# Kernel optimization log

Hardware: AMD Instinct MI355X
Metric: run time of the kernel (lower is better)

The kernel has to match this reference:

```python
import jax, jax.numpy as jnp
import numpy as np

H, W = 512, 512
K = 10
N_ACTIONS = 8
HID1, HID2, HIDP = 32, 64, 32
# 8-neighborhood directions (i_dot, j_dot), as in env.DIRS
DIRS = [(-1, -1), (-1, 0), (-1, 1), (0, -1), (0, 1), (1, -1), (1, 0), (1, 1)]


def setup_inputs() -> dict:
    key = jax.random.key(0)
    ks = jax.random.split(key, 16)
    n_state = H * W
    w = lambda k, shape: (jax.random.normal(k, shape, dtype=jnp.float32) * 0.02)
    return {
        "x": jax.random.uniform(ks[0], (3, H, W), dtype=jnp.float32),
        "pos": jax.random.randint(ks[1], (2,), 0, H, dtype=jnp.int32),
        "W1": w(ks[2], (HID1, 3 * n_state)), "b1": jnp.zeros((HID1,), jnp.float32),
        "W2": w(ks[3], (HID2, HID1)), "b2": jnp.zeros((HID2,), jnp.float32),
        "Wro": w(ks[4], (n_state, HID2)), "bro": jnp.zeros((n_state,), jnp.float32),
        "Wri": w(ks[5], (n_state, HID2)), "bri": jnp.zeros((n_state,), jnp.float32),
        "Wp": w(ks[6], (n_state, HID2)), "bp": jnp.zeros((n_state,), jnp.float32),
        "Wpol": w(ks[7], (HIDP, 4 * n_state)), "bpol": jnp.zeros((HIDP,), jnp.float32),
        "Whead": w(ks[8], (N_ACTIONS, HIDP)), "bhead": jnp.zeros((N_ACTIONS,), jnp.float32),
    }


def reference(x, pos, W1, b1, W2, b2, Wro, bro, Wri, bri, Wp, bp, Wpol, bpol, Whead, bhead):
    state = x.reshape(-1)  # (3*H*W,)
    h = jax.nn.relu(W1 @ state + b1)
    h = jax.nn.relu(W2 @ h + b2)
    r_out = jax.nn.sigmoid(Wro @ h + bro).reshape(H, W)
    r_in = jax.nn.sigmoid(Wri @ h + bri).reshape(H, W)
    p = jax.nn.sigmoid(Wp @ h + bp).reshape(H, W)

    p_pad = jnp.pad(p, 1)
    rin_pad = jnp.pad(r_in, 1)
    rout_pad = jnp.pad(r_out, 1)

    def step(v, _):
        v_pad = jnp.pad(v, 1)  # (H+2, W+2)
        cands = []
        for i_dot, j_dot in DIRS:
            xs = j_dot + 1  # note: original code uses j_dot along axis 0
            ys = i_dot + 1
            cands.append(
                v_pad[xs:xs + H, ys:ys + W] * p_pad[xs:xs + H, ys:ys + W]
                + rin_pad[xs:xs + H, ys:ys + W] - rout_pad[xs:xs + H, ys:ys + W]
            )
        return jnp.max(jnp.stack(cands, 0), axis=0), None

    v, _ = jax.lax.scan(step, jnp.zeros((H, W), jnp.float32), None, length=K)

    inp_pol = jnp.concatenate([v.reshape(-1), state])  # (4*H*W,)
    logits = Whead @ jax.nn.relu(Wpol @ inp_pol + bpol) + bhead
    action_prob = jax.nn.softmax(logits, axis=-1)
    state_value = v[pos[0], pos[1]]
    return action_prob, state_value
```

## Files before the change

kernel.cpp:

```cpp
#include <hip/hip_runtime.h>

#define HW 512
#define NSTATE (HW * HW)
#define NC4_X 196608
#define NC4_POLROW 262144
#define NC4_V 65536

#define CH4 1024
#define NCH_X 192

#define WS_PART1 0
#define WS_PARTP 6144
#define WS_H2 14336
#define WS_DRO 16384
#define WS_DRI 278528
#define WS_DP 540672
#define WS_V 802816

#define SGB __builtin_amdgcn_sched_group_barrier

typedef float f4v __attribute__((ext_vector_type(4)));

__device__ __forceinline__ float wred(float a) {
  a += __shfl_xor(a, 32);
  a += __shfl_xor(a, 16);
  a += __shfl_xor(a, 8);
  a += __shfl_xor(a, 4);
  a += __shfl_xor(a, 2);
  a += __shfl_xor(a, 1);
  return a;
}

__device__ __forceinline__ float span_dot(const float4* __restrict__ wp,
                                          const float4* __restrict__ xp) {
  float acc = 0.f;
#pragma unroll
  for (int bt = 0; bt < 2; ++bt) {
    float4 w[8], xv[8];
#pragma unroll
    for (int j = 0; j < 8; ++j) w[j] = wp[bt * 512 + j * 64];
#pragma unroll
    for (int j = 0; j < 8; ++j) xv[j] = xp[bt * 512 + j * 64];
    SGB(0x020, 16, 0);
#pragma unroll
    for (int j = 0; j < 8; ++j)
      acc += w[j].x * xv[j].x + w[j].y * xv[j].y + w[j].z * xv[j].z +
             w[j].w * xv[j].w;
  }
  return acc;
}

__global__ __launch_bounds__(256) void mv_w1(const float4* __restrict__ W1,
                                             const float4* __restrict__ x,
                                             float* __restrict__ part1) {
  int b = blockIdx.x;
  int row = b / 48, cb = b - row * 48;
  int tid = threadIdx.x, wave = tid >> 6, lane = tid & 63;
  int ch = cb * 4 + wave;
  const float4* __restrict__ wp =
      W1 + (size_t)row * NC4_X + (size_t)ch * CH4 + lane;
  const float4* __restrict__ xp = x + (size_t)ch * CH4 + lane;
  float acc = span_dot(wp, xp);
  acc = wred(acc);
  if (lane == 0) part1[ch * 32 + row] = acc;
}

__global__ __launch_bounds__(1024) void finish_h(
    const float* __restrict__ partials, const float* __restrict__ b1,
    const float* __restrict__ W2, const float* __restrict__ b2,
    float* __restrict__ h2out) {
  __shared__ float red[32][32];
  __shared__ float h1[32];
  int tid = threadIdx.x;
  int row = tid & 31, grp = tid >> 5;
  float s = 0.f;
  for (int b = grp; b < NCH_X; b += 32) s += partials[b * 32 + row];
  red[grp][row] = s;
  __syncthreads();
  if (tid < 32) {
    float t = b1[tid];
    for (int g = 0; g < 32; ++g) t += red[g][tid];
    h1[tid] = fmaxf(t, 0.f);
  }
  __syncthreads();
  if (tid < 64) {
    float t = b2[tid];
    for (int k = 0; k < 32; ++k) t += W2[tid * 32 + k] * h1[k];
    h2out[tid] = fmaxf(t, 0.f);
  }
}

__device__ __forceinline__ void issue16(const float4* __restrict__ wp,
                                        f4v* w) {
  const float* a0 = (const float*)(wp);
  const float* a1 = (const float*)(wp + 256);
  const float* a2 = (const float*)(wp + 512);
  const float* a3 = (const float*)(wp + 768);
  asm volatile(
      "global_load_dwordx4 %0, %16, off nt\n\t"
      "global_load_dwordx4 %1, %16, off offset:1024 nt\n\t"
      "global_load_dwordx4 %2, %16, off offset:2048 nt\n\t"
      "global_load_dwordx4 %3, %16, off offset:3072 nt\n\t"
      "global_load_dwordx4 %4, %17, off nt\n\t"
      "global_load_dwordx4 %5, %17, off offset:1024 nt\n\t"
      "global_load_dwordx4 %6, %17, off offset:2048 nt\n\t"
      "global_load_dwordx4 %7, %17, off offset:3072 nt\n\t"
      "global_load_dwordx4 %8, %18, off nt\n\t"
      "global_load_dwordx4 %9, %18, off offset:1024 nt\n\t"
      "global_load_dwordx4 %10, %18, off offset:2048 nt\n\t"
      "global_load_dwordx4 %11, %18, off offset:3072 nt\n\t"
      "global_load_dwordx4 %12, %19, off nt\n\t"
      "global_load_dwordx4 %13, %19, off offset:1024 nt\n\t"
      "global_load_dwordx4 %14, %19, off offset:2048 nt\n\t"
      "global_load_dwordx4 %15, %19, off offset:3072 nt"
      : "=&v"(w[0]), "=&v"(w[1]), "=&v"(w[2]), "=&v"(w[3]), "=&v"(w[4]),
        "=&v"(w[5]), "=&v"(w[6]), "=&v"(w[7]), "=&v"(w[8]), "=&v"(w[9]),
        "=&v"(w[10]), "=&v"(w[11]), "=&v"(w[12]), "=&v"(w[13]), "=&v"(w[14]),
        "=&v"(w[15])
      : "v"(a0), "v"(a1), "v"(a2), "v"(a3)
      : "memory");
}

__device__ __forceinline__ void consume16(const f4v* w, float4 h4, int wave,
                                          int lane, float (*dots)[64],
                                          float* __restrict__ Dst) {
  float part[16];
#pragma unroll
  for (int j = 0; j < 16; ++j)
    part[j] = w[j][0] * h4.x + w[j][1] * h4.y + w[j][2] * h4.z + w[j][3] * h4.w;
#pragma unroll
  for (int j = 0; j < 16; ++j) {
    part[j] += __shfl_xor(part[j], 8);
    part[j] += __shfl_xor(part[j], 4);
    part[j] += __shfl_xor(part[j], 2);
    part[j] += __shfl_xor(part[j], 1);
  }
  int k = lane & 15, grp = lane >> 4;
  if (k == 0) {
#pragma unroll
    for (int j = 0; j < 16; ++j) dots[wave][j * 4 + grp] = part[j];
  }
  asm volatile("s_waitcnt lgkmcnt(0)" ::: "memory");
  __builtin_amdgcn_sched_barrier(0);
  Dst[lane] = dots[wave][lane];
}

#define VMW16 do { asm volatile("s_waitcnt vmcnt(16)" ::: "memory"); \
                   __builtin_amdgcn_sched_barrier(0); } while (0)
#define VMW0 do { asm volatile("s_waitcnt vmcnt(0)" ::: "memory"); \
                  __builtin_amdgcn_sched_barrier(0); } while (0)

__global__ __launch_bounds__(256, 2) void rop_part(
    const float4* __restrict__ Wro4, const float4* __restrict__ Wri4,
    const float4* __restrict__ Wp4, const float* __restrict__ h2,
    float* __restrict__ dro, float* __restrict__ dri,
    float* __restrict__ dp) {
  __shared__ float dots[4][64];
  int tid = threadIdx.x, wave = tid >> 6, lane = tid & 63;
  int gw = blockIdx.x * 4 + wave;
  float4 h4 = ((const float4*)h2)[lane & 15];
  const float4* __restrict__ p0 = Wro4 + (size_t)gw * CH4 + lane;
  const float4* __restrict__ p1 = Wri4 + (size_t)gw * CH4 + lane;
  const float4* __restrict__ p2 = Wp4 + (size_t)gw * CH4 + lane;
  f4v A[16], B[16];
  issue16(p0, A);
  issue16(p1, B);
  VMW16;
  consume16(A, h4, wave, lane, dots, dro + (size_t)gw * 64);
  issue16(p2, A);
  VMW16;
  consume16(B, h4, wave, lane, dots, dri + (size_t)gw * 64);
  VMW0;
  consume16(A, h4, wave, lane, dots, dp + (size_t)gw * 64);
}

#define VTILE 16
#define VHALO 10
#define ULW 44
#define ULH 38
__device__ __forceinline__ void row_win(const float* __restrict__ r,
                                        float e[6]) {
  float4 L = *reinterpret_cast<const float4*>(r - 4);
  float4 M = *reinterpret_cast<const float4*>(r);
  float4 R = *reinterpret_cast<const float4*>(r + 4);
  e[0] = L.w; e[1] = M.x; e[2] = M.y; e[3] = M.z; e[4] = M.w; e[5] = R.x;
}
__global__ __launch_bounds__(384) void valiter_kernel(
    const float* __restrict__ dro, const float* __restrict__ dri,
    const float* __restrict__ dp, const float* __restrict__ bro,
    const float* __restrict__ bri, const float* __restrict__ bp,
    float* __restrict__ vout) {
  __shared__ float ua[ULH * ULW];
  __shared__ float ub[ULH * ULW];
  int tid = threadIdx.x;
  int blk = blockIdx.x;
  int ti = blk >> 5, tj = blk & 31;
  for (int idx = tid; idx < ULH * ULW; idx += 384) {
    ua[idx] = 0.f;
    ub[idx] = 0.f;
  }
  int i = tid / 9, j4 = tid - i * 9;
  bool active = (i < 36);
  int cb = 4 + 4 * j4;
  float pp[4], rr[4];
  if (active) {
    int gi = ti * VTILE - VHALO + i;
    int gj0 = tj * VTILE - VHALO + 4 * j4;
#pragma unroll
    for (int k = 0; k < 4; ++k) {
      int gj = gj0 + k;
      bool ok = (gi >= 0) & (gi < HW) & (gj >= 0) & (gj < HW);
      if (ok) {
        int g = gi * HW + gj;
        float sro = 1.f / (1.f + __expf(-(dro[g] + bro[g])));
        float sri = 1.f / (1.f + __expf(-(dri[g] + bri[g])));
        pp[k] = 1.f / (1.f + __expf(-(dp[g] + bp[g])));
        rr[k] = sri - sro;
      } else {
        pp[k] = 0.f;
        rr[k] = 0.f;
      }
    }
  }
  __syncthreads();
  if (active) {
    *reinterpret_cast<float4*>(&ua[(i + 1) * ULW + cb]) =
        make_float4(rr[0], rr[1], rr[2], rr[3]);
  }
  __syncthreads();
  float* src = ua;
  float* dst = ub;
  for (int q = 0; q < 9; ++q) {
    int lo = q + 1, hi = 35 - q;
    if (active && i >= lo && i < hi && (4 * j4 + 4) > lo && (4 * j4) < hi) {
      float eA[6], eB[6], eC[6];
      row_win(src + i * ULW + cb, eA);
      row_win(src + (i + 1) * ULW + cb, eB);
      row_win(src + (i + 2) * ULW + cb, eC);
      float res[4];
#pragma unroll
      for (int k = 0; k < 4; ++k) {
        float a = fmaxf(fmaxf(eA[k], eA[k + 1]), eA[k + 2]);
        float c = fmaxf(fmaxf(eC[k], eC[k + 1]), eC[k + 2]);
        float b = fmaxf(eB[k], eB[k + 2]);
        float m = fmaxf(fmaxf(a, c), b);
        res[k] = m * pp[k] + rr[k];
      }
      *reinterpret_cast<float4*>(&dst[(i + 1) * ULW + cb]) =
          make_float4(res[0], res[1], res[2], res[3]);
    }
    __syncthreads();
    float* t_ = src;
    src = dst;
    dst = t_;
  }
  if (active && i >= 10 && i < 26 && (4 * j4 + 4) > 10 && (4 * j4) < 26) {
    float eA[6], eB[6], eC[6];
    row_win(src + i * ULW + cb, eA);
    row_win(src + (i + 1) * ULW + cb, eB);
    row_win(src + (i + 2) * ULW + cb, eC);
#pragma unroll
    for (int k = 0; k < 4; ++k) {
      int cj = 4 * j4 + k;
      if (cj >= 10 && cj < 26) {
        float a = fmaxf(fmaxf(eA[k], eA[k + 1]), eA[k + 2]);
        float c = fmaxf(fmaxf(eC[k], eC[k + 1]), eC[k + 2]);
        float b = fmaxf(eB[k], eB[k + 2]);
        float m = fmaxf(fmaxf(a, c), b);
        vout[(ti * VTILE + i - 10) * HW + tj * VTILE + cj - 10] = m;
      }
    }
  }
}

__global__ __launch_bounds__(256) void mv_pol(const float4* __restrict__ Wpol,
                                              const float4* __restrict__ x,
                                              const float4* __restrict__ v,
                                              float* __restrict__ partP) {
  int b = blockIdx.x;
  int tid = threadIdx.x, wave = tid >> 6, lane = tid & 63;
  int f = b * 4 + wave;
  int row = f >> 8, rc = f & 255;
  const float4* __restrict__ wp = Wpol + (size_t)f * CH4 + lane;
  const float4* __restrict__ xp =
      (rc < 64) ? (v + (size_t)rc * CH4 + lane)
                : (x + (size_t)(rc - 64) * CH4 + lane);
  float acc = span_dot(wp, xp);
  acc = wred(acc);
  if (lane == 0) partP[rc * 32 + row] = acc;
}

__global__ __launch_bounds__(1024) void finish_pol(
    const float* __restrict__ partP, const float* __restrict__ bpol,
    const float* __restrict__ Whead, const float* __restrict__ bhead,
    const float* __restrict__ v, const int* __restrict__ pos,
    float* __restrict__ out) {
  __shared__ float red[32][32];
  __shared__ float hp[32];
  __shared__ float logits[8];
  int tid = threadIdx.x;
  int row = tid & 31, grp = tid >> 5;
  float s = 0.f;
  for (int b = grp; b < 256; b += 32) s += partP[b * 32 + row];
  red[grp][row] = s;
  __syncthreads();
  if (tid < 32) {
    float t = bpol[tid];
    for (int g = 0; g < 32; ++g) t += red[g][tid];
    hp[tid] = fmaxf(t, 0.f);
  }
  __syncthreads();
  if (tid < 8) {
    float t = bhead[tid];
    for (int k = 0; k < 32; ++k) t += Whead[tid * 32 + k] * hp[k];
    logits[tid] = t;
  }
  __syncthreads();
  if (tid == 0) {
    float mx = logits[0];
    for (int j = 1; j < 8; ++j) mx = fmaxf(mx, logits[j]);
    float e[8], sum = 0.f;
    for (int j = 0; j < 8; ++j) {
      e[j] = __expf(logits[j] - mx);
      sum += e[j];
    }
    for (int j = 0; j < 8; ++j) out[j] = e[j] / sum;
    out[8] = v[pos[0] * HW + pos[1]];
  }
}

extern "C" void kernel_launch(void* const* d_in, const int* in_sizes, int n_in,
                              void* d_out, int out_size, void* d_ws,
                              size_t ws_size, hipStream_t stream) {
  const float* x = (const float*)d_in[0];
  const int* pos = (const int*)d_in[1];
  const float* W1 = (const float*)d_in[2];
  const float* b1 = (const float*)d_in[3];
  const float* W2 = (const float*)d_in[4];
  const float* b2 = (const float*)d_in[5];
  const float* Wro = (const float*)d_in[6];
  const float* bro = (const float*)d_in[7];
  const float* Wri = (const float*)d_in[8];
  const float* bri = (const float*)d_in[9];
  const float* Wp = (const float*)d_in[10];
  const float* bp = (const float*)d_in[11];
  const float* Wpol = (const float*)d_in[12];
  const float* bpol = (const float*)d_in[13];
  const float* Whead = (const float*)d_in[14];
  const float* bhead = (const float*)d_in[15];
  float* ws = (float*)d_ws;
  float* out = (float*)d_out;

  float* part1 = ws + WS_PART1;
  float* partP = ws + WS_PARTP;
  float* h2 = ws + WS_H2;
  float* drob = ws + WS_DRO;
  float* drib = ws + WS_DRI;
  float* dpb = ws + WS_DP;
  float* vbuf = ws + WS_V;

  mv_w1<<<1536, 256, 0, stream>>>((const float4*)W1, (const float4*)x, part1);
  finish_h<<<1, 1024, 0, stream>>>(part1, b1, W2, b2, h2);
  rop_part<<<1024, 256, 0, stream>>>((const float4*)Wro, (const float4*)Wri,
                                     (const float4*)Wp, h2, drob, drib, dpb);
  valiter_kernel<<<1024, 384, 0, stream>>>(drob, drib, dpb, bro, bri, bp,
                                           vbuf);
  mv_pol<<<2048, 256, 0, stream>>>((const float4*)Wpol, (const float4*)x,
                                   (const float4*)vbuf, partP);
  finish_pol<<<1, 1024, 0, stream>>>(partP, bpol, Whead, bhead, vbuf, pos,
                                     out);
}
```

Baseline: 105.1 us.

## Split policy matvec by input, fuse x-part into rop kernel with sigmoid epilogue

The policy matvec's state (x) portion does not depend on the value iteration, so it now runs in the same launch as the Wro/Wri/Wp matvec, interleaved by block index. Only the v-dependent quarter runs after value iteration. The sigmoids and bias adds move into the rop kernel epilogue, which writes only p and r_in-r_out. Value iteration therefore reads two halo-overlapping planes instead of six and skips repeated exp work on halo cells. The combined kernel mixes two workloads with different register and occupancy profiles.

```diff
diff --git a/kernel.cpp b/kernel.cpp
--- a/kernel.cpp
+++ b/kernel.cpp
@@ -8,14 +8,14 @@
 
 #define CH4 1024
 #define NCH_X 192
+#define NCH_V 64
 
 #define WS_PART1 0
 #define WS_PARTP 6144
 #define WS_H2 14336
-#define WS_DRO 16384
-#define WS_DRI 278528
-#define WS_DP 540672
-#define WS_V 802816
+#define WS_P 14400
+#define WS_RD (WS_P + NSTATE)
+#define WS_V (WS_RD + NSTATE)
 
 #define SGB __builtin_amdgcn_sched_group_barrier
 
@@ -122,8 +122,8 @@
 }
 
 __device__ __forceinline__ void consume16(const f4v* w, float4 h4, int wave,
-                                          int lane, float (*dots)[64],
-                                          float* __restrict__ Dst) {
+                                          int m, int lane,
+                                          float (*dots)[3][64]) {
   float part[16];
 #pragma unroll
   for (int j = 0; j < 16; ++j)
@@ -138,11 +138,8 @@
   int k = lane & 15, grp = lane >> 4;
   if (k == 0) {
 #pragma unroll
-    for (int j = 0; j < 16; ++j) dots[wave][j * 4 + grp] = part[j];
-  }
-  asm volatile("s_waitcnt lgkmcnt(0)" ::: "memory");
-  __builtin_amdgcn_sched_barrier(0);
-  Dst[lane] = dots[wave][lane];
+    for (int j = 0; j < 16; ++j) dots[wave][m][j * 4 + grp] = part[j];
+  }
 }
 
 #define VMW16 do { asm volatile("s_waitcnt vmcnt(16)" ::: "memory"); \
@@ -150,14 +147,30 @@
 #define VMW0 do { asm volatile("s_waitcnt vmcnt(0)" ::: "memory"); \
                   __builtin_amdgcn_sched_barrier(0); } while (0)
 
-__global__ __launch_bounds__(256, 2) void rop_part(
+__global__ __launch_bounds__(256, 2) void ropx(
     const float4* __restrict__ Wro4, const float4* __restrict__ Wri4,
     const float4* __restrict__ Wp4, const float* __restrict__ h2,
-    float* __restrict__ dro, float* __restrict__ dri,
-    float* __restrict__ dp) {
-  __shared__ float dots[4][64];
+    const float* __restrict__ bro, const float* __restrict__ bri,
+    const float* __restrict__ bp, float* __restrict__ p_out,
+    float* __restrict__ rd_out, const float4* __restrict__ Wpol,
+    const float4* __restrict__ x, float* __restrict__ partP) {
+  __shared__ float dots[4][3][64];
   int tid = threadIdx.x, wave = tid >> 6, lane = tid & 63;
-  int gw = blockIdx.x * 4 + wave;
+  int b5 = blockIdx.x / 5, m5 = blockIdx.x - b5 * 5;
+  if (m5 >= 2) {
+    int xblk = b5 * 3 + (m5 - 2);
+    int row = xblk / 48, cb = xblk - row * 48;
+    int ch = cb * 4 + wave;
+    const float4* __restrict__ wp =
+        Wpol + (size_t)row * NC4_POLROW + NC4_V + (size_t)ch * CH4 + lane;
+    const float4* __restrict__ xp = x + (size_t)ch * CH4 + lane;
+    float acc = span_dot(wp, xp);
+    acc = wred(acc);
+    if (lane == 0) partP[(64 + ch) * 32 + row] = acc;
+    return;
+  }
+  int rblk = b5 * 2 + m5;
+  int gw = rblk * 4 + wave;
   float4 h4 = ((const float4*)h2)[lane & 15];
   const float4* __restrict__ p0 = Wro4 + (size_t)gw * CH4 + lane;
   const float4* __restrict__ p1 = Wri4 + (size_t)gw * CH4 + lane;
@@ -166,12 +179,23 @@
   issue16(p0, A);
   issue16(p1, B);
   VMW16;
-  consume16(A, h4, wave, lane, dots, dro + (size_t)gw * 64);
+  consume16(A, h4, wave, 0, lane, dots);
   issue16(p2, A);
   VMW16;
-  consume16(B, h4, wave, lane, dots, dri + (size_t)gw * 64);
+  consume16(B, h4, wave, 1, lane, dots);
   VMW0;
-  consume16(A, h4, wave, lane, dots, dp + (size_t)gw * 64);
+  consume16(A, h4, wave, 2, lane, dots);
+  asm volatile("s_waitcnt lgkmcnt(0)" ::: "memory");
+  __builtin_amdgcn_sched_barrier(0);
+  int o = gw * 64 + lane;
+  float dro = dots[wave][0][lane] + bro[o];
+  float dri = dots[wave][1][lane] + bri[o];
+  float dp = dots[wave][2][lane] + bp[o];
+  float sro = 1.f / (1.f + __expf(-dro));
+  float sri = 1.f / (1.f + __expf(-dri));
+  float pv = 1.f / (1.f + __expf(-dp));
+  p_out[o] = pv;
+  rd_out[o] = sri - sro;
 }
 
 #define VTILE 16
@@ -186,9 +210,7 @@
   e[0] = L.w; e[1] = M.x; e[2] = M.y; e[3] = M.z; e[4] = M.w; e[5] = R.x;
 }
 __global__ __launch_bounds__(384) void valiter_kernel(
-    const float* __restrict__ dro, const float* __restrict__ dri,
-    const float* __restrict__ dp, const float* __restrict__ bro,
-    const float* __restrict__ bri, const float* __restrict__ bp,
+    const float* __restrict__ p, const float* __restrict__ rd,
     float* __restrict__ vout) {
   __shared__ float ua[ULH * ULW];
   __shared__ float ub[ULH * ULW];
@@ -210,16 +232,9 @@
     for (int k = 0; k < 4; ++k) {
       int gj = gj0 + k;
       bool ok = (gi >= 0) & (gi < HW) & (gj >= 0) & (gj < HW);
-      if (ok) {
-        int g = gi * HW + gj;
-        float sro = 1.f / (1.f + __expf(-(dro[g] + bro[g])));
-        float sri = 1.f / (1.f + __expf(-(dri[g] + bri[g])));
-        pp[k] = 1.f / (1.f + __expf(-(dp[g] + bp[g])));
-        rr[k] = sri - sro;
-      } else {
-        pp[k] = 0.f;
-        rr[k] = 0.f;
-      }
+      int gidx = gi * HW + gj;
+      pp[k] = ok ? p[gidx] : 0.f;
+      rr[k] = ok ? rd[gidx] : 0.f;
     }
   }
   __syncthreads();
@@ -273,21 +288,19 @@
   }
 }
 
-__global__ __launch_bounds__(256) void mv_pol(const float4* __restrict__ Wpol,
-                                              const float4* __restrict__ x,
-                                              const float4* __restrict__ v,
-                                              float* __restrict__ partP) {
+__global__ __launch_bounds__(256) void mv_polv(const float4* __restrict__ Wpol,
+                                               const float4* __restrict__ v,
+                                               float* __restrict__ partP) {
   int b = blockIdx.x;
+  int row = b / 16, cb = b - row * 16;
   int tid = threadIdx.x, wave = tid >> 6, lane = tid & 63;
-  int f = b * 4 + wave;
-  int row = f >> 8, rc = f & 255;
-  const float4* __restrict__ wp = Wpol + (size_t)f * CH4 + lane;
-  const float4* __restrict__ xp =
-      (rc < 64) ? (v + (size_t)rc * CH4 + lane)
-                : (x + (size_t)(rc - 64) * CH4 + lane);
+  int ch = cb * 4 + wave;
+  const float4* __restrict__ wp =
+      Wpol + (size_t)row * NC4_POLROW + (size_t)ch * CH4 + lane;
+  const float4* __restrict__ xp = v + (size_t)ch * CH4 + lane;
   float acc = span_dot(wp, xp);
   acc = wred(acc);
-  if (lane == 0) partP[rc * 32 + row] = acc;
+  if (lane == 0) partP[ch * 32 + row] = acc;
 }
 
 __global__ __launch_bounds__(1024) void finish_pol(
@@ -354,19 +367,19 @@
   float* part1 = ws + WS_PART1;
   float* partP = ws + WS_PARTP;
   float* h2 = ws + WS_H2;
-  float* drob = ws + WS_DRO;
-  float* drib = ws + WS_DRI;
-  float* dpb = ws + WS_DP;
+  float* pbuf = ws + WS_P;
+  float* rdbuf = ws + WS_RD;
   float* vbuf = ws + WS_V;
 
   mv_w1<<<1536, 256, 0, stream>>>((const float4*)W1, (const float4*)x, part1);
   finish_h<<<1, 1024, 0, stream>>>(part1, b1, W2, b2, h2);
-  rop_part<<<1024, 256, 0, stream>>>((const float4*)Wro, (const float4*)Wri,
-                                     (const float4*)Wp, h2, drob, drib, dpb);
-  valiter_kernel<<<1024, 384, 0, stream>>>(drob, drib, dpb, bro, bri, bp,
-                                           vbuf);
-  mv_pol<<<2048, 256, 0, stream>>>((const float4*)Wpol, (const float4*)x,
-                                   (const float4*)vbuf, partP);
+  ropx<<<2560, 256, 0, stream>>>((const float4*)Wro, (const float4*)Wri,
+                                 (const float4*)Wp, h2, bro, bri, bp, pbuf,
+                                 rdbuf, (const float4*)Wpol, (const float4*)x,
+                                 partP);
+  valiter_kernel<<<1024, 384, 0, stream>>>(pbuf, rdbuf, vbuf);
+  mv_polv<<<512, 256, 0, stream>>>((const float4*)Wpol, (const float4*)vbuf,
+                                   partP);
   finish_pol<<<1, 1024, 0, stream>>>(partP, bpol, Whead, bhead, vbuf, pos,
                                      out);
 }
```

Result: faster. 100.9 us (-4.0%).
